# Kernel tuning notes

Hardware: AMD Instinct MI355X
Metric: run time of the kernel (lower is better)

The kernel has to match this reference:

```python
import jax, jax.numpy as jnp
import numpy as np

EPS = 1e-5
CLIP = 1.0

@jax.custom_vjp
def ste_sign(x):
    return jnp.sign(x)

def _ste_fwd(x):
    return jnp.sign(x), x

def _ste_bwd(x, g):
    return (g * (jnp.abs(x) <= CLIP).astype(g.dtype),)

ste_sign.defvjp(_ste_fwd, _ste_bwd)

def conv2d(x, w, stride, pad):
    return jax.lax.conv_general_dilated(
        x, w, window_strides=(stride, stride), padding=[(pad, pad), (pad, pad)],
        dimension_numbers=('NCHW', 'OIHW', 'NCHW'))

def bn(x, g, b, m, v):
    inv = g / jnp.sqrt(v + EPS)
    return x * inv[None, :, None, None] + (b - m * inv)[None, :, None, None]

def setup_inputs() -> dict:
    key = jax.random.key(0)
    ks = jax.random.split(key, 16)
    def rn(k, shape, scale=0.05):
        return jax.random.normal(k, shape, dtype=jnp.float32) * scale
    C = [64, 128, 128, 192, 192]
    d = {}
    d['x'] = jax.random.normal(ks[0], (128, 1, 128, 128), dtype=jnp.float32)
    d['conv1_w'] = rn(ks[1], (C[0], 1, 3, 3), 0.3)
    d['conv1_b'] = rn(ks[2], (C[0],))
    d['w2'] = rn(ks[3], (C[1], C[0], 3, 3), 0.3)
    d['w3'] = rn(ks[4], (C[2], C[1], 3, 3), 0.3)
    d['w4'] = rn(ks[5], (C[3], C[2], 3, 3), 0.3)
    d['w5'] = rn(ks[6], (C[4], C[3], 1, 1), 0.3)
    d['conv6_w'] = rn(ks[7], (12, C[4], 1, 1), 0.1)
    d['conv6_b'] = rn(ks[8], (12,))
    d['fc_w'] = rn(ks[9], (12, 12), 0.2)
    d['fc_b'] = rn(ks[10], (12,))
    for i, c in enumerate(C):
        kk = jax.random.split(jax.random.fold_in(key, 100 + i), 4)
        d[f'bn{i+1}_g'] = 1.0 + rn(kk[0], (c,), 0.1)
        d[f'bn{i+1}_b'] = rn(kk[1], (c,), 0.1)
        d[f'bn{i+1}_m'] = rn(kk[2], (c,), 0.1)
        d[f'bn{i+1}_v'] = 1.0 + jnp.abs(rn(kk[3], (c,), 0.1))
    return d

def reference(x, conv1_w, conv1_b, w2, w3, w4, w5, conv6_w, conv6_b, fc_w, fc_b,
              bn1_g, bn1_b, bn1_m, bn1_v, bn2_g, bn2_b, bn2_m, bn2_v,
              bn3_g, bn3_b, bn3_m, bn3_v, bn4_g, bn4_b, bn4_m, bn4_v,
              bn5_g, bn5_b, bn5_m, bn5_v):
    # conv1 (float) + BN + ReLU
    h = conv2d(x, conv1_w, 2, 1) + conv1_b[None, :, None, None]
    h = jax.nn.relu(bn(h, bn1_g, bn1_b, bn1_m, bn1_v))
    # binarized conv blocks: sign(activation) conv sign(weight)
    h = conv2d(ste_sign(h), ste_sign(w2), 1, 1)
    h = jax.nn.relu(bn(h, bn2_g, bn2_b, bn2_m, bn2_v))
    h = conv2d(ste_sign(h), ste_sign(w3), 2, 1)
    h = jax.nn.relu(bn(h, bn3_g, bn3_b, bn3_m, bn3_v))
    h = conv2d(ste_sign(h), ste_sign(w4), 1, 1)
    h = jax.nn.relu(bn(h, bn4_g, bn4_b, bn4_m, bn4_v))
    h = conv2d(ste_sign(h), ste_sign(w5), 1, 0)
    h = jax.nn.relu(bn(h, bn5_g, bn5_b, bn5_m, bn5_v))
    # 1x1 conv to classes, global average pool, FC, softmax
    h = conv2d(h, conv6_w, 1, 0) + conv6_b[None, :, None, None]
    h = jnp.mean(h, axis=(2, 3))  # [B, num_classes]
    logits = h @ fc_w.T + fc_b
    return jax.nn.softmax(logits, axis=1)
```

## Files before the change

### kernel.cpp

```cpp
#include <hip/hip_runtime.h>
#include <cstdint>

using u64 = unsigned long long;
using u32 = unsigned int;
typedef __attribute__((ext_vector_type(4))) int int4v;

struct PrepArgs {
  const float* bng[5]; const float* bnb[5]; const float* bnm[5]; const float* bnv[5];
  float* inv1; float* cc1; float* inv5; float* cc5;
  int* thr[3]; int* flp[3];
  const float* w[4];
  u64* wp[4]; u64* wz[4];
  u32* flags;
};

__global__ __launch_bounds__(256) void prep_all(PrepArgs a) {
  int i = blockIdx.x * 256 + threadIdx.x;
  if (i < 704) {
    const int off[6] = {0, 64, 192, 320, 512, 704};
    int l = 0;
    while (i >= off[l + 1]) ++l;
    int c = i - off[l];
    float iv = __fdiv_rn(a.bng[l][c], __fsqrt_rn(__fadd_rn(a.bnv[l][c], 1e-5f)));
    float cb = __fsub_rn(a.bnb[l][c], __fmul_rn(a.bnm[l][c], iv));
    if (l == 0) { a.inv1[c] = iv; a.cc1[c] = cb; }
    else if (l == 4) { a.inv5[c] = iv; a.cc5[c] = cb; }
    else {
      auto pred = [&](int v_) {
        return __fadd_rn(__fmul_rn((float)v_, iv), cb) > 0.f;
      };
      int Tx, fl;
      if (iv == 0.f) { Tx = pred(0) ? -100000 : 100000; fl = 0; }
      else if (iv > 0.f) {
        if (pred(-2048)) { Tx = -100000; fl = 0; }
        else if (!pred(2048)) { Tx = 100000; fl = 0; }
        else {
          int lo = -2048, hi = 2048;
          while (hi - lo > 1) { int md = (lo + hi) >> 1; if (pred(md)) hi = md; else lo = md; }
          Tx = hi; fl = 0;
        }
      } else {
        if (pred(2048)) { Tx = -100000; fl = -1; }
        else if (!pred(-2048)) { Tx = 100000; fl = -1; }
        else {
          int lo = -2048, hi = 2048;
          while (hi - lo > 1) { int md = (lo + hi) >> 1; if (pred(md)) lo = md; else hi = md; }
          Tx = lo ^ -1; fl = -1;
        }
      }
      a.thr[l - 1][c] = Tx; a.flp[l - 1][c] = fl;
    }
    return;
  }
  int j = i - 704;
  if (j >= 7488) return;
  const int poff[5] = {0, 1152, 3456, 6912, 7488};
  const int ICt[4] = {64, 128, 128, 192};
  const int Kt[4]  = {9, 9, 9, 1};
  const int Wt[4]  = {1, 2, 2, 3};
  int l = 0;
  while (j >= poff[l + 1]) ++l;
  int idx = j - poff[l];
  int W = Wt[l], K = Kt[l], IC = ICt[l];
  int wi = idx % W;
  int rest = idx / W;
  int t = rest % K;
  int oc = rest / K;
  u64 p = 0, z = 0;
  int icbase = wi * 64;
  int nb = IC - icbase; if (nb > 64) nb = 64;
  const float* w = a.w[l];
  for (int b = 0; b < nb; ++b) {
    float f = w[((size_t)oc * IC + (icbase + b)) * K + t];
    if (f > 0.f) p |= (1ull << b);
    else if (f == 0.f) z |= (1ull << b);
  }
  a.wp[l][idx] = p;
  a.wz[l][idx] = z;
  if (z) atomicOr(a.flags + l, 1u);
}

template <int CINW, int COUT>
__global__ __launch_bounds__(256) void prep_bfrag(const float* __restrict__ w,
                                                  signed char* __restrict__ bf) {
  constexpr int NKC = 9 * CINW;
  constexpr int NT = COUT / 16;
  constexpr int CIN = 64 * CINW;
  int idx = blockIdx.x * 256 + threadIdx.x;
  if (idx >= NT * NKC * 64) return;
  int lane = idx & 63;
  int rest = idx >> 6;
  int kc = rest % NKC;
  int t = rest / NKC;
  int tap = kc / CINW, wd = kc % CINW;
  int n = t * 16 + (lane & 15);
  int icb = wd * 64 + (lane >> 4) * 16;
  signed char* dst = bf + (size_t)idx * 16;
#pragma unroll
  for (int i = 0; i < 16; ++i) {
    float f = w[((size_t)n * CIN + icb + i) * 9 + tap];
    dst[i] = (f > 0.f) ? 1 : ((f < 0.f) ? -1 : 0);
  }
}

__global__ __launch_bounds__(256) void pad_x(const float* __restrict__ x,
                                             float* __restrict__ xpad) {
  int idx = blockIdx.x * 256 + threadIdx.x;
  int c = idx & 127, r = (idx >> 7) & 127, n = idx >> 14;
  xpad[((size_t)n * 130 + r + 1) * 136 + c + 1] = x[idx];
}

__global__ __launch_bounds__(256) void conv1_bin(
    const float* __restrict__ xpad, const float* __restrict__ w1, const float* __restrict__ b1,
    const float* __restrict__ inv1, const float* __restrict__ cc1,
    u64* __restrict__ a1p) {
  int tid = threadIdx.x, lane = tid & 63;
  int rb = __builtin_amdgcn_readfirstlane(tid >> 6);
  int blk = blockIdx.x;
  int y = (blk % 16) * 4 + rb;
  int n = blk / 16;
  float W[9];
#pragma unroll
  for (int t = 0; t < 9; ++t) W[t] = w1[lane * 9 + t];
  float bias = b1[lane], iv = inv1[lane], cb = cc1[lane];
  const float* sb = xpad + ((size_t)n * 130 + 2 * y) * 136;
  float A[12], B[12], C[12];
  u64 rowm = 0;
  int xb = 0;

#define FLD(BUF, POFF)                                     \
  _Pragma("unroll") for (int _r = 0; _r < 3; ++_r)         \
  _Pragma("unroll") for (int _j = 0; _j < 4; ++_j)         \
    BUF[_r * 4 + _j] = sb[_r * 136 + (POFF) + _j];
#define FPX(XO, B0F, C0, B1F, C1, B2F, C2) {                          \
  float acc = 0.f;                                                    \
  _Pragma("unroll") for (int _r = 0; _r < 3; ++_r)                    \
    acc += B0F[_r * 4 + (C0)] * W[_r * 3 + 0]                         \
         + B1F[_r * 4 + (C1)] * W[_r * 3 + 1]                         \
         + B2F[_r * 4 + (C2)] * W[_r * 3 + 2];                        \
  float h = __fadd_rn(acc, bias);                                     \
  float bnv = __fadd_rn(__fmul_rn(h, iv), cb);                        \
  u64 _m = __ballot(bnv > 0.f);                                       \
  rowm = (lane == (XO)) ? _m : rowm; }
#define FSTEP(BA, BB, BC, POFF, XB)  \
  FLD(BC, (POFF) + 8);               \
  FPX((XB), BA, 0, BA, 1, BA, 2);    \
  FPX((XB) + 1, BA, 2, BA, 3, BB, 0);

  FLD(A, 0); FLD(B, 4);
  for (int g = 0; g < 10; ++g) {
    FSTEP(A, B, C, 0, xb);
    FSTEP(B, C, A, 4, xb + 2);
    FSTEP(C, A, B, 8, xb + 4);
    sb += 12; xb += 6;
  }
  FSTEP(A, B, C, 0, xb);
  FSTEP(B, C, A, 4, xb + 2);
  a1p[((size_t)n * 66 + (y + 1)) * 68 + lane + 1] = rowm;
#undef FLD
#undef FPX
#undef FSTEP
}

template <int CINW, int COUT, int STRIDE, int IN_HW, int OUT_HW, int MT, int TSTG, int OPAD>
__global__ __launch_bounds__(256) void bconv_mfma(
    const u64* __restrict__ ain, const signed char* __restrict__ bf,
    const int* __restrict__ thr, const int* __restrict__ flp,
    u64* __restrict__ aout) {
  constexpr int IPW = IN_HW + 4;
  constexpr int NKC = 9 * CINW;
  constexpr int NT = COUT / 16;
  constexpr int NSTG = NT / TSTG;
  constexpr int OCW = (COUT + 63) / 64;
  constexpr int XG = OUT_HW / (16 * MT);
  constexpr int FRAG = TSTG * NKC * 64;
  constexpr int CPT = (FRAG + 255) / 256;
  constexpr int NW32 = NT / 2;
  __shared__ int4v bs[FRAG];

  int tid = threadIdx.x, lane = tid & 63;
  int wv = __builtin_amdgcn_readfirstlane(tid >> 6);
  int pos = blockIdx.x * 4 + wv;
  int xg = pos % XG;
  int rest = pos / XG;
  int y = rest % OUT_HW;
  int n = rest / OUT_HW;
  int m = lane & 15;
  int kg = lane >> 4;

  const int4v* bfv = (const int4v*)bf;

  int4v breg[CPT];
#pragma unroll
  for (int i = 0; i < CPT; ++i) {
    int ix = tid + i * 256;
    if (FRAG % 256 == 0 || ix < FRAG) breg[i] = bfv[ix];
  }

  int4v af[MT * NKC];
#pragma unroll
  for (int mt = 0; mt < MT; ++mt) {
    int x = (xg * MT + mt) * 16 + m;
    const u64* abase = ain + (((size_t)n * (IN_HW + 2) + STRIDE * y) * IPW
                              + (size_t)STRIDE * x) * CINW;
#pragma unroll
    for (int dy = 0; dy < 3; ++dy)
#pragma unroll
      for (int dx = 0; dx < 3; ++dx)
#pragma unroll
        for (int wd = 0; wd < CINW; ++wd) {
          u64 aw = abase[((size_t)dy * IPW + dx) * CINW + wd];
          u32 t16 = (u32)(aw >> (kg * 16)) & 0xFFFFu;
          int4v v;
          v.x = (int)((((t16      ) & 0xFu) * 0x00204081u) & 0x01010101u);
          v.y = (int)((((t16 >> 4 ) & 0xFu) * 0x00204081u) & 0x01010101u);
          v.z = (int)((((t16 >> 8 ) & 0xFu) * 0x00204081u) & 0x01010101u);
          v.w = (int)((((t16 >> 12) & 0xFu) * 0x00204081u) & 0x01010101u);
          af[mt * NKC + (dy * 3 + dx) * CINW + wd] = v;
        }
  }

  u32 acc32[MT][NW32];
#pragma unroll
  for (int mt = 0; mt < MT; ++mt)
#pragma unroll
    for (int wl = 0; wl < NW32; ++wl) acc32[mt][wl] = 0;

#pragma unroll
  for (int s = 0; s < NSTG; ++s) {
    __syncthreads();
#pragma unroll
    for (int i = 0; i < CPT; ++i) {
      int ix = tid + i * 256;
      if (FRAG % 256 == 0 || ix < FRAG) bs[ix] = breg[i];
    }
    __syncthreads();
    if (s + 1 < NSTG) {
      const int4v* src = bfv + (size_t)(s + 1) * FRAG;
#pragma unroll
      for (int i = 0; i < CPT; ++i) {
        int ix = tid + i * 256;
        if (FRAG % 256 == 0 || ix < FRAG) breg[i] = src[ix];
      }
    }
#pragma unroll
    for (int tl = 0; tl < TSTG; ++tl) {
      constexpr int dummy = 0; (void)dummy;
      int4v c[MT];
#pragma unroll
      for (int mt = 0; mt < MT; ++mt) c[mt] = (int4v){0, 0, 0, 0};
#pragma unroll
      for (int kc = 0; kc < NKC; ++kc) {
        int4v bb = bs[(tl * NKC + kc) * 64 + lane];
#pragma unroll
        for (int mt = 0; mt < MT; ++mt)
          c[mt] = __builtin_amdgcn_mfma_i32_16x16x64_i8(af[mt * NKC + kc], bb, c[mt], 0, 0, 0);
      }
      const int t = s * TSTG + tl;
      int tx = thr[t * 16 + m];
      int fl = flp[t * 16 + m];
#pragma unroll
      for (int mt = 0; mt < MT; ++mt) {
        u64 b0 = __ballot((c[mt].x ^ fl) >= tx);
        u64 b1 = __ballot((c[mt].y ^ fl) >= tx);
        u64 b2 = __ballot((c[mt].z ^ fl) >= tx);
        u64 b3 = __ballot((c[mt].w ^ fl) >= tx);
        u64 s01 = (m & 1) ? b1 : b0;
        u64 s23 = (m & 1) ? b3 : b2;
        u64 bsel = (m & 2) ? s23 : s01;
        u32 slice = (u32)(bsel >> ((m >> 2) * 16)) & 0xFFFFu;
        acc32[mt][t >> 1] |= slice << ((t & 1) * 16);
      }
    }
  }

  if (kg == 0) {
    u32* out32 = (u32*)aout;
#pragma unroll
    for (int mt = 0; mt < MT; ++mt) {
      int x = (xg * MT + mt) * 16 + m;
      size_t px32;
      if (OPAD)
        px32 = (((size_t)n * (OUT_HW + 2) + (y + 1)) * (OUT_HW + 4) + (x + 1)) * (OCW * 2);
      else
        px32 = (((size_t)n * OUT_HW + y) * OUT_HW + x) * (OCW * 2);
#pragma unroll
      for (int wl = 0; wl < NW32; ++wl)
        out32[px32 + wl] = acc32[mt][wl];
    }
  }
}

#define NCH5 8
__global__ __launch_bounds__(192) void bconv5_pool(
    const u64* __restrict__ ain, const u64* __restrict__ wp, const u64* __restrict__ wz,
    const u32* __restrict__ flag, const float* __restrict__ inv5, const float* __restrict__ cc5,
    float* __restrict__ partial) {
  int n = blockIdx.x / NCH5, ch = blockIdx.x % NCH5;
  int oc = threadIdx.x;
  u64 W0 = wp[oc * 3], W1 = wp[oc * 3 + 1], W2 = wp[oc * 3 + 2];
  bool anyz = (*flag != 0u);
  float iv = inv5[oc], cb = cc5[oc];
  const u64* sb = ain + ((size_t)n * 1024 + ch * 128) * 3;
  u64 A0, A1, A2, B0, B1, B2, C0, C1, C2;
  float acc = 0.f;
#define LD5(P, a0_, a1_, a2_) { a0_ = sb[(P) * 3]; a1_ = sb[(P) * 3 + 1]; a2_ = sb[(P) * 3 + 2]; }
#define PX5(a0_, a1_, a2_) {                                                   \
  int _pa = __popcll(a0_) + __popcll(a1_) + __popcll(a2_);                     \
  int _s = __popcll(a0_ & W0) + __popcll(a1_ & W1) + __popcll(a2_ & W2);       \
  int _val = 2 * _s - _pa;                                                     \
  if (anyz) _val += __popcll(a0_ & wz[oc * 3]) + __popcll(a1_ & wz[oc * 3 + 1])\
                  + __popcll(a2_ & wz[oc * 3 + 2]);                            \
  float _b = __fadd_rn(__fmul_rn((float)_val, iv), cb);                        \
  acc += fmaxf(_b, 0.f); }
  LD5(0, A0, A1, A2); LD5(1, B0, B1, B2);
  for (int g = 0; g < 42; ++g) {
    LD5(2, C0, C1, C2); PX5(A0, A1, A2);
    LD5(3, A0, A1, A2); PX5(B0, B1, B2);
    LD5(4, B0, B1, B2); PX5(C0, C1, C2);
    sb += 9;
  }
  PX5(A0, A1, A2); PX5(B0, B1, B2);
  partial[((size_t)n * NCH5 + ch) * 192 + oc] = acc;
#undef LD5
#undef PX5
}

__global__ __launch_bounds__(192) void head2(
    const float* __restrict__ partial,
    const float* __restrict__ w6, const float* __restrict__ b6,
    const float* __restrict__ fw, const float* __restrict__ fb,
    float* __restrict__ out) {
  __shared__ float pool_s[192];
  __shared__ float h6s[12];
  __shared__ float lgs[12];
  int n = blockIdx.x, t = threadIdx.x;
  float s = 0.f;
#pragma unroll
  for (int ch = 0; ch < NCH5; ++ch) s += partial[((size_t)n * NCH5 + ch) * 192 + t];
  pool_s[t] = s;
  __syncthreads();
  if (t < 12) {
    float a = 0.f;
    for (int c = 0; c < 192; ++c) a += pool_s[c] * w6[t * 192 + c];
    h6s[t] = b6[t] + a * (1.0f / 1024.0f);
  }
  __syncthreads();
  if (t < 12) {
    float s2 = fb[t];
    for (int k = 0; k < 12; ++k) s2 += h6s[k] * fw[t * 12 + k];
    lgs[t] = s2;
  }
  __syncthreads();
  if (t == 0) {
    float mx = -1e30f;
    for (int j = 0; j < 12; ++j) mx = fmaxf(mx, lgs[j]);
    float e[12], se = 0.f;
    for (int j = 0; j < 12; ++j) { e[j] = expf(lgs[j] - mx); se += e[j]; }
    for (int j = 0; j < 12; ++j) out[n * 12 + j] = e[j] / se;
  }
}

extern "C" void kernel_launch(void* const* d_in, const int* in_sizes, int n_in,
                              void* d_out, int out_size, void* d_ws, size_t ws_size,
                              hipStream_t stream) {
  const float* x   = (const float*)d_in[0];
  const float* w1  = (const float*)d_in[1];
  const float* b1  = (const float*)d_in[2];
  const float* w2  = (const float*)d_in[3];
  const float* w3  = (const float*)d_in[4];
  const float* w4  = (const float*)d_in[5];
  const float* w5  = (const float*)d_in[6];
  const float* w6  = (const float*)d_in[7];
  const float* b6  = (const float*)d_in[8];
  const float* fcw = (const float*)d_in[9];
  const float* fcb = (const float*)d_in[10];
  float* out = (float*)d_out;

  char* ws = (char*)d_ws;
  size_t off = 0;
  auto alloc = [&](size_t bytes) -> void* {
    void* p = ws + off;
    off += (bytes + 255) & ~(size_t)255;
    return p;
  };
  size_t xp_sz = (size_t)128 * 130 * 136 * 4;
  size_t a1_sz = (size_t)128 * 66 * 68 * 1 * 8;
  size_t a2_sz = (size_t)128 * 66 * 68 * 2 * 8;
  size_t a3_sz = (size_t)128 * 34 * 36 * 2 * 8;
  float* xpad = (float*)alloc(xp_sz);
  u64* a1p = (u64*)alloc(a1_sz);
  u64* a2p = (u64*)alloc(a2_sz);
  u64* a3p = (u64*)alloc(a3_sz);
  size_t zero_sz = xp_sz + a1_sz + a2_sz + a3_sz;
  u64* a4p = (u64*)alloc((size_t)128 * 32 * 32 * 3 * 8);
  float* partial = (float*)alloc((size_t)128 * NCH5 * 192 * 4);
  float* inv1 = (float*)alloc(64 * 4);
  float* cc1  = (float*)alloc(64 * 4);
  float* inv5 = (float*)alloc(192 * 4);
  float* cc5  = (float*)alloc(192 * 4);
  int* thr2 = (int*)alloc(128 * 4); int* flp2 = (int*)alloc(128 * 4);
  int* thr3 = (int*)alloc(128 * 4); int* flp3 = (int*)alloc(128 * 4);
  int* thr4 = (int*)alloc(192 * 4); int* flp4 = (int*)alloc(192 * 4);
  u64* wp2 = (u64*)alloc(128 * 9 * 1 * 8);
  u64* wz2 = (u64*)alloc(128 * 9 * 1 * 8);
  u64* wp3 = (u64*)alloc(128 * 9 * 2 * 8);
  u64* wz3 = (u64*)alloc(128 * 9 * 2 * 8);
  u64* wp4 = (u64*)alloc(192 * 9 * 2 * 8);
  u64* wz4 = (u64*)alloc(192 * 9 * 2 * 8);
  u64* wp5 = (u64*)alloc(192 * 1 * 3 * 8);
  u64* wz5 = (u64*)alloc(192 * 1 * 3 * 8);
  u32* flags = (u32*)alloc(4 * sizeof(u32));
  signed char* bf2 = (signed char*)alloc((size_t)8 * 9 * 64 * 16);
  signed char* bf3 = (signed char*)alloc((size_t)8 * 18 * 64 * 16);
  signed char* bf4 = (signed char*)alloc((size_t)12 * 18 * 64 * 16);
  (void)ws_size; (void)n_in; (void)in_sizes; (void)out_size;

  hipMemsetAsync(xpad, 0, zero_sz, stream);
  hipMemsetAsync(flags, 0, 4 * sizeof(u32), stream);

  PrepArgs pa;
  for (int l = 0; l < 5; ++l) {
    pa.bng[l] = (const float*)d_in[11 + 4 * l + 0];
    pa.bnb[l] = (const float*)d_in[11 + 4 * l + 1];
    pa.bnm[l] = (const float*)d_in[11 + 4 * l + 2];
    pa.bnv[l] = (const float*)d_in[11 + 4 * l + 3];
  }
  pa.inv1 = inv1; pa.cc1 = cc1; pa.inv5 = inv5; pa.cc5 = cc5;
  pa.thr[0] = thr2; pa.flp[0] = flp2;
  pa.thr[1] = thr3; pa.flp[1] = flp3;
  pa.thr[2] = thr4; pa.flp[2] = flp4;
  pa.w[0] = w2; pa.w[1] = w3; pa.w[2] = w4; pa.w[3] = w5;
  pa.wp[0] = wp2; pa.wp[1] = wp3; pa.wp[2] = wp4; pa.wp[3] = wp5;
  pa.wz[0] = wz2; pa.wz[1] = wz3; pa.wz[2] = wz4; pa.wz[3] = wz5;
  pa.flags = flags;
  prep_all<<<32, 256, 0, stream>>>(pa);

  prep_bfrag<1, 128><<<(8 * 9 * 64 + 255) / 256, 256, 0, stream>>>(w2, bf2);
  prep_bfrag<2, 128><<<(8 * 18 * 64 + 255) / 256, 256, 0, stream>>>(w3, bf3);
  prep_bfrag<2, 192><<<(12 * 18 * 64 + 255) / 256, 256, 0, stream>>>(w4, bf4);

  pad_x<<<(128 * 128 * 128) / 256, 256, 0, stream>>>(x, xpad);

  conv1_bin<<<128 * 16, 256, 0, stream>>>(xpad, w1, b1, inv1, cc1, a1p);

  bconv_mfma<1, 128, 1, 64, 64, 2, 2, 1><<<4096, 256, 0, stream>>>(
      a1p, bf2, thr2, flp2, a2p);

  bconv_mfma<2, 128, 2, 64, 32, 1, 1, 1><<<2048, 256, 0, stream>>>(
      a2p, bf3, thr3, flp3, a3p);

  bconv_mfma<2, 192, 1, 32, 32, 1, 1, 0><<<2048, 256, 0, stream>>>(
      a3p, bf4, thr4, flp4, a4p);

  bconv5_pool<<<128 * NCH5, 192, 0, stream>>>(a4p, wp5, wz5, flags + 3, inv5, cc5, partial);

  head2<<<128, 192, 0, stream>>>(partial, w6, b6, fcw, fcb, out);
}
```

Before: 224.0 us.

## Use 32x32x32 int8 MFMA for second binary conv layer

Replaces the generic 16x16x64 MFMA kernel for layer 2 with a dedicated kernel built on the 32x32x32 int8 MFMA. Weight fragments are repacked by a new prep kernel. All weights go into LDS once per block, with no staging loop, and thresholded output bits are gathered via ballots into 32-bit words per 32 output channels. The goal is more work per MFMA and less LDS/stage synchronisation, at the cost of higher register and LDS use (occupancy 2 blocks) and a more complex output bit-packing.

```diff
diff --git a/kernel.cpp b/kernel.cpp
--- a/kernel.cpp
+++ b/kernel.cpp
@@ -4,6 +4,7 @@
 using u64 = unsigned long long;
 using u32 = unsigned int;
 typedef __attribute__((ext_vector_type(4))) int int4v;
+typedef __attribute__((ext_vector_type(16))) int int16v;
 
 struct PrepArgs {
   const float* bng[5]; const float* bnb[5]; const float* bnm[5]; const float* bnv[5];
@@ -103,6 +104,26 @@
   }
 }
 
+__global__ __launch_bounds__(256) void prep_bfrag32(const float* __restrict__ w,
+                                                    signed char* __restrict__ bf) {
+  int idx = blockIdx.x * 256 + threadIdx.x;
+  if (idx >= 4 * 18 * 64) return;
+  int lane = idx & 63;
+  int rest = idx >> 6;
+  int s = rest % 18;
+  int t = rest / 18;
+  int oc = t * 32 + (lane & 31);
+  int kbase = s * 32 + (lane >> 5) * 16;
+  signed char* dst = bf + (size_t)idx * 16;
+#pragma unroll
+  for (int i = 0; i < 16; ++i) {
+    int k = kbase + i;
+    int ch = k & 63, tap = k >> 6;
+    float f = w[((size_t)oc * 64 + ch) * 9 + tap];
+    dst[i] = (f > 0.f) ? 1 : ((f < 0.f) ? -1 : 0);
+  }
+}
+
 __global__ __launch_bounds__(256) void pad_x(const float* __restrict__ x,
                                              float* __restrict__ xpad) {
   int idx = blockIdx.x * 256 + threadIdx.x;
@@ -162,6 +183,78 @@
 #undef FSTEP
 }
 
+__global__ __launch_bounds__(256, 2) void bconv2_32(
+    const u64* __restrict__ ain, const signed char* __restrict__ bf,
+    const int* __restrict__ thr, const int* __restrict__ flp,
+    u64* __restrict__ aout) {
+  __shared__ int4v bs[4 * 18 * 64];
+  int tid = threadIdx.x, lane = tid & 63;
+  int wv = __builtin_amdgcn_readfirstlane(tid >> 6);
+  int pos = blockIdx.x * 4 + wv;
+  int xg = pos & 1;
+  int y = (pos >> 1) & 63;
+  int n = pos >> 7;
+  int ln31 = lane & 31;
+  int kg16 = (lane >> 5) * 16;
+  int px = xg * 32 + ln31;
+
+  const int4v* bfv = (const int4v*)bf;
+  int4v breg[18];
+#pragma unroll
+  for (int i = 0; i < 18; ++i) breg[i] = bfv[tid + i * 256];
+
+  const u64* abase = ain + ((size_t)n * 66 + y) * 68 + px;
+  int4v af[18];
+#pragma unroll
+  for (int tap = 0; tap < 9; ++tap) {
+    int dy = tap / 3, dx = tap % 3;
+    u64 aw = abase[(size_t)dy * 68 + dx];
+#pragma unroll
+    for (int h = 0; h < 2; ++h) {
+      u32 t16 = (u32)(aw >> (h * 32 + kg16)) & 0xFFFFu;
+      int4v v;
+      v.x = (int)((((t16      ) & 0xFu) * 0x00204081u) & 0x01010101u);
+      v.y = (int)((((t16 >> 4 ) & 0xFu) * 0x00204081u) & 0x01010101u);
+      v.z = (int)((((t16 >> 8 ) & 0xFu) * 0x00204081u) & 0x01010101u);
+      v.w = (int)((((t16 >> 12) & 0xFu) * 0x00204081u) & 0x01010101u);
+      af[tap * 2 + h] = v;
+    }
+  }
+
+  int txv[4], flv[4];
+#pragma unroll
+  for (int t = 0; t < 4; ++t) { txv[t] = thr[t * 32 + ln31]; flv[t] = flp[t * 32 + ln31]; }
+
+#pragma unroll
+  for (int i = 0; i < 18; ++i) bs[tid + i * 256] = breg[i];
+  __syncthreads();
+
+  u32* out32 = (u32*)aout;
+#pragma unroll
+  for (int t = 0; t < 4; ++t) {
+    int16v c = {0, 0, 0, 0, 0, 0, 0, 0, 0, 0, 0, 0, 0, 0, 0, 0};
+#pragma unroll
+    for (int s = 0; s < 18; ++s) {
+      int4v bb = bs[(t * 18 + s) * 64 + lane];
+      c = __builtin_amdgcn_mfma_i32_32x32x32_i8(af[s], bb, c, 0, 0, 0);
+    }
+    int tx = txv[t], fl = flv[t];
+    u32 oww = 0;
+#pragma unroll
+    for (int r = 0; r < 16; ++r) {
+      int plo = (r & 3) + 8 * (r >> 2);
+      u64 bal = __ballot((c[r] ^ fl) >= tx);
+      u32 wlo = (u32)bal, whi = (u32)(bal >> 32);
+      oww = (lane == plo) ? wlo : oww;
+      oww = (lane == plo + 4) ? whi : oww;
+    }
+    if (lane < 32) {
+      int x = xg * 32 + lane;
+      out32[(((size_t)n * 66 + (y + 1)) * 68 + (x + 1)) * 4 + t] = oww;
+    }
+  }
+}
+
 template <int CINW, int COUT, int STRIDE, int IN_HW, int OUT_HW, int MT, int TSTG, int OPAD>
 __global__ __launch_bounds__(256) void bconv_mfma(
     const u64* __restrict__ ain, const signed char* __restrict__ bf,
@@ -245,7 +338,6 @@
     }
 #pragma unroll
     for (int tl = 0; tl < TSTG; ++tl) {
-      constexpr int dummy = 0; (void)dummy;
       int4v c[MT];
 #pragma unroll
       for (int mt = 0; mt < MT; ++mt) c[mt] = (int4v){0, 0, 0, 0};
@@ -411,7 +503,7 @@
   u64* wp5 = (u64*)alloc(192 * 1 * 3 * 8);
   u64* wz5 = (u64*)alloc(192 * 1 * 3 * 8);
   u32* flags = (u32*)alloc(4 * sizeof(u32));
-  signed char* bf2 = (signed char*)alloc((size_t)8 * 9 * 64 * 16);
+  signed char* bf2x = (signed char*)alloc((size_t)4 * 18 * 64 * 16);
   signed char* bf3 = (signed char*)alloc((size_t)8 * 18 * 64 * 16);
   signed char* bf4 = (signed char*)alloc((size_t)12 * 18 * 64 * 16);
   (void)ws_size; (void)n_in; (void)in_sizes; (void)out_size;
@@ -436,7 +528,7 @@
   pa.flags = flags;
   prep_all<<<32, 256, 0, stream>>>(pa);
 
-  prep_bfrag<1, 128><<<(8 * 9 * 64 + 255) / 256, 256, 0, stream>>>(w2, bf2);
+  prep_bfrag32<<<18, 256, 0, stream>>>(w2, bf2x);
   prep_bfrag<2, 128><<<(8 * 18 * 64 + 255) / 256, 256, 0, stream>>>(w3, bf3);
   prep_bfrag<2, 192><<<(12 * 18 * 64 + 255) / 256, 256, 0, stream>>>(w4, bf4);
 
@@ -444,8 +536,7 @@
 
   conv1_bin<<<128 * 16, 256, 0, stream>>>(xpad, w1, b1, inv1, cc1, a1p);
 
-  bconv_mfma<1, 128, 1, 64, 64, 2, 2, 1><<<4096, 256, 0, stream>>>(
-      a1p, bf2, thr2, flp2, a2p);
+  bconv2_32<<<4096, 256, 0, stream>>>(a1p, bf2x, thr2, flp2, a2p);
 
   bconv_mfma<2, 128, 2, 64, 32, 1, 1, 1><<<2048, 256, 0, stream>>>(
       a2p, bf3, thr3, flp3, a3p);
```

New measurement: 216.7 us. -3.3%, faster.
